# Optimization experiments

Measured on AMD Instinct MI355X. Metric: run time of the kernel, lower is better.

The kernel has to match this reference:

```python
import math
import jax, jax.numpy as jnp
import numpy as np

N_HEAD = 4
D_MODEL = 96
BS, N_TOK = 32, 512
A2LEN = 150          # a2len % 16 != 0 so padn > 0 (asserted in torch code)
DST_MXLEN = 32


def setup_inputs() -> dict:
    key = jax.random.key(0)
    k1, k2, k3, k4, k5, k6 = jax.random.split(key, 6)
    x = jax.random.normal(k1, (BS, N_TOK, D_MODEL), dtype=jnp.float32)
    # LinearM: w is [outdim, indim+1], last column is the bias, zeroed at init
    wqv_w = 0.02 * jax.random.normal(k2, (3 * D_MODEL, D_MODEL + 1), dtype=jnp.float32)
    wqv_w = wqv_w.at[:, -1].set(0.0)
    fanout_w = 0.02 * jax.random.normal(k3, (D_MODEL, D_MODEL + 1), dtype=jnp.float32)
    fanout_w = fanout_w.at[:, -1].set(0.0)

    def make_coo(k):
        # COO triples [dst, src, dst_cnt]; every dst has DST_MXLEN sources
        dst = jnp.repeat(jnp.arange(N_TOK), DST_MXLEN)
        src = jax.random.randint(k, (N_TOK * DST_MXLEN,), 0, N_TOK)
        cnt = jnp.tile(jnp.arange(DST_MXLEN), N_TOK)
        return jnp.stack([dst, src, cnt], axis=1).astype(jnp.int32)

    coo0 = make_coo(k4)
    coo1 = make_coo(k5)
    a2a = jnp.sort(jax.random.permutation(k6, N_TOK)[:A2LEN]).astype(jnp.int32)
    return {"x": x, "wqv_w": wqv_w, "fanout_w": fanout_w,
            "coo0": coo0, "coo1": coo1, "a2a": a2a, "dst_mxlen": DST_MXLEN}


def _linm(w, x):
    # LinearM: einsum('oi,bhi->bho') + bias column
    return jnp.einsum('oi,bti->bto', w[:, :-1], x) + w[:, -1]


def _l1attn_sparse(v, q, k, coo, dst_mxlen):
    # l1attn_sparse_cuda.L1AttnSparse: per-(dst,src) L1 scores scattered into a
    # [n_tok, dst_mxlen] ragged table (pad = -1e12), softmax over the fan-in slot.
    bs, n_tok, h, w = q.shape
    dst, src, cnt = coo[:, 0], coo[:, 1], coo[:, 2]
    scale = 1.0 / math.sqrt(w)
    ww = -jnp.sum(jnp.abs(q[:, dst] - k[:, src]), axis=-1) * scale    # [bs, cl, h]
    attn = jnp.full((bs, n_tok, dst_mxlen, h), -1e12, dtype=q.dtype)
    attn = attn.at[:, dst, cnt, :].set(ww)
    attn_sm = jax.nn.softmax(attn, axis=2)
    vw = jnp.zeros((bs, n_tok, dst_mxlen, h, w), dtype=q.dtype)
    vw = vw.at[:, dst, cnt, :, :].set(v[:, src])                      # gather by src
    return jnp.einsum('bdrh,bdrhw->bdhw', attn_sm, vw)


def _forward(x, wqv_w, fanout_w, coo0, coo1, a2a, dst_mxlen):
    bs, n_tok, width = x.shape
    h = N_HEAD
    y = _linm(wqv_w, x)
    q, k, v = jnp.split(y, 3, axis=-1)

    # --- dense all-to-all L1 attention on tokens a2a, channels 72:96 (h*6) ---
    a2len = a2a.shape[0]
    q1 = q[:, a2a, 72:].reshape(bs, a2len, h, 6)
    k1 = k[:, a2a, 72:].reshape(bs, a2len, h, 6)
    v1 = v[:, a2a, 72:].reshape(bs, a2len, h, 6)
    padl = (a2len + 15) // 16 * 16
    q2 = jnp.pad(q1, ((0, 0), (0, padl - a2len), (0, 0), (0, 0)))
    k2 = jnp.pad(k1, ((0, 0), (0, padl - a2len), (0, 0), (0, 0)))
    scale = 1.0 / math.sqrt(6)
    # l1attn_cuda.L1Attn: a[b, s, d, h] = -scale * sum_w |q[b,d,h,w] - k[b,s,h,w]|
    a = -jnp.sum(jnp.abs(q2[:, None, :, :, :] - k2[:, :, None, :, :]), axis=-1) * scale
    a = a[:, :a2len + 1, :a2len + 1, :]   # keep one zero-score pad row (attention sink)
    a = jax.nn.softmax(a, axis=1)         # softmax over src dim
    a = a[:, :a2len, :a2len, :]
    b1 = jnp.einsum('bsdh,bshw->bdhw', a, v1)
    b2 = jnp.zeros((bs, n_tok, h, 6), dtype=x.dtype).at[:, a2a].set(b1)
    dense = b2.reshape(bs, n_tok, h * 6)

    # --- two sparse COO L1-attention groups: channels 32:52 and 52:72 (h*5) ---
    sparse_out = []
    for i, coo in enumerate((coo0, coo1)):
        sta = 32 + 20 * i
        q1 = q[:, :, sta:sta + 20].reshape(bs, n_tok, h, 5)
        k1 = k[:, :, sta:sta + 20].reshape(bs, n_tok, h, 5)
        v1 = v[:, :, sta:sta + 20].reshape(bs, n_tok, h, 5)
        sparse_out.append(_l1attn_sparse(v1, q1, k1, coo, dst_mxlen).reshape(bs, n_tok, h * 5))

    # channels 0:32 are never written -> zeros
    b = jnp.concatenate([jnp.zeros((bs, n_tok, 32), dtype=x.dtype),
                         sparse_out[0], sparse_out[1], dense], axis=-1)
    yb = b * jax.nn.sigmoid(1.702 * b)    # QuickGELU
    return x + _linm(fanout_w, yb)


def reference(x, wqv_w, fanout_w, coo0, coo1, a2a, dst_mxlen):
    return _forward(x, wqv_w, fanout_w, coo0, coo1, a2a, dst_mxlen)
```

## Files before the change

### kernel.cpp

```cpp
#include <hip/hip_runtime.h>
#include <hip/hip_bf16.h>
#include <math.h>

#define BS    32
#define T     512
#define BT    (BS * T)
#define D     96
#define H     4
#define MX    32
#define A2MAX 160

#define QKV_TOK  16
#define FUSE_TOK 16

__device__ __forceinline__ int a2a_pos(const int* __restrict__ a2a, int n, int t) {
    int lo = 0, hi = n;
    while (lo < hi) { const int mid = (lo + hi) >> 1; if (a2a[mid] < t) lo = mid + 1; else hi = mid; }
    return (lo < n && a2a[lo] == t) ? lo : -1;
}

__global__ void prep_kernel(const float* __restrict__ wqv, const float* __restrict__ fw,
                            const int* __restrict__ coo0, const int* __restrict__ coo1,
                            int nedges,
                            float* __restrict__ WT, float* __restrict__ FWT,
                            int* __restrict__ srcs) {
    int idx = blockIdx.x * blockDim.x + threadIdx.x;
    if (idx < 97 * 192) {
        const int i = idx / 192, oc = idx - 192 * i;
        const int p = oc >> 6, c = oc & 63;
        WT[idx] = wqv[(p * 96 + 32 + c) * 97 + i];
        return;
    }
    idx -= 97 * 192;
    if (idx < 65 * 96) {
        const int i = idx / 96, o = idx - 96 * i;
        FWT[idx] = fw[o * 97 + 32 + i];
        return;
    }
    idx -= 65 * 96;
    if (idx < 2 * nedges) {
        const int ci = idx / nedges;
        const int e  = idx - ci * nedges;
        const int* row = (ci == 0 ? coo0 : coo1) + e * 3;
        const int dst = row[0], src = row[1], cnt = row[2];
        if (dst >= 0 && dst < T && cnt >= 0 && cnt < MX)
            srcs[(ci * T + dst) * MX + cnt] = src;
    }
}

__global__ void qkv_kernel(const float* __restrict__ x, const float* __restrict__ WT,
                           const int* __restrict__ a2a, int a2len,
                           float* __restrict__ QS, float* __restrict__ KS,
                           float* __restrict__ VS,
                           float* __restrict__ Qg, float* __restrict__ Kg,
                           float* __restrict__ Vg) {
    const int tid  = threadIdx.x;
    const int base = blockIdx.x * QKV_TOK;
    const int tloc = base & (T - 1);
    __shared__ float xs[QKV_TOK * D];
    __shared__ int   posA[QKV_TOK];
    float4* xs4 = (float4*)xs;
    const float4* xg = (const float4*)(x + base * D);
    xs4[tid]       = xg[tid];
    xs4[tid + 192] = xg[tid + 192];
    if (tid < QKV_TOK) posA[tid] = a2a_pos(a2a, a2len, tloc + tid);
    __syncthreads();
    float acc[QKV_TOK];
    const float bias = WT[96 * 192 + tid];
    #pragma unroll
    for (int j = 0; j < QKV_TOK; ++j) acc[j] = bias;
    #pragma unroll 3
    for (int i4 = 0; i4 < 24; ++i4) {
        const float w0 = WT[(4 * i4 + 0) * 192 + tid];
        const float w1 = WT[(4 * i4 + 1) * 192 + tid];
        const float w2 = WT[(4 * i4 + 2) * 192 + tid];
        const float w3 = WT[(4 * i4 + 3) * 192 + tid];
        #pragma unroll
        for (int j = 0; j < QKV_TOK; ++j) {
            const float4 xv = xs4[j * 24 + i4];
            acc[j] += w0 * xv.x + w1 * xv.y + w2 * xv.z + w3 * xv.w;
        }
    }
    const int part = tid >> 6, c = tid & 63;
    const int b    = base >> 9;
    if (c < 40) {
        float* XS = (part == 0) ? QS : (part == 1 ? KS : VS);
        float4* dp = (float4*)(XS + ((size_t)c * BS + b) * T + tloc);
        #pragma unroll
        for (int m = 0; m < 4; ++m)
            dp[m] = make_float4(acc[4 * m], acc[4 * m + 1],
                                acc[4 * m + 2], acc[4 * m + 3]);
    } else {
        float* g = (part == 0) ? Qg : (part == 1 ? Kg : Vg);
        #pragma unroll
        for (int j = 0; j < QKV_TOK; ++j) {
            const int ps = posA[j];
            if (ps >= 0) g[((size_t)b * A2MAX + ps) * 24 + (c - 40)] = acc[j];
        }
    }
}

__global__ void attn_kernel(const float* __restrict__ QS, const float* __restrict__ KS,
                            const float* __restrict__ VS, const int* __restrict__ srcs,
                            const float* __restrict__ Qg, const float* __restrict__ Kg,
                            const float* __restrict__ Vg, const int* __restrict__ a2a,
                            int a2len, int extra, float* __restrict__ B) {
    __shared__ float sm[A2MAX * 32 * 2];
    __shared__ int   rows[A2MAX];
    const int b   = blockIdx.y;
    const int tid = threadIdx.x;

    if (blockIdx.x < 8) {
        const int ci = blockIdx.x >> 2, h = blockIdx.x & 3;
        const int cb = 20 * ci + 5 * h;
        float* ks = sm;
        float* vs = sm + 5 * T;
        const size_t rowbase = ((size_t)cb * BS + b) * T;
        #pragma unroll
        for (int i = tid; i < 5 * T; i += 512) {
            const int w = i >> 9, s = i & (T - 1);
            ks[i] = KS[rowbase + (size_t)w * BS * T + s];
            vs[i] = VS[rowbase + (size_t)w * BS * T + s];
        }
        __syncthreads();
        const float iscale = 0.4472135954999579f;
        const int t = tid;
        const float q0 = QS[rowbase + 0 * BS * T + t];
        const float q1 = QS[rowbase + 1 * BS * T + t];
        const float q2 = QS[rowbase + 2 * BS * T + t];
        const float q3 = QS[rowbase + 3 * BS * T + t];
        const float q4 = QS[rowbase + 4 * BS * T + t];
        const int4* sp4 = (const int4*)(srcs + (ci * T + t) * MX);
        float l = 0.f, o0 = 0.f, o1 = 0.f, o2 = 0.f, o3 = 0.f, o4 = 0.f;
        #pragma unroll 2
        for (int c4 = 0; c4 < MX / 4; ++c4) {
            const int4 s4 = sp4[c4];
            const int sv[4] = {s4.x, s4.y, s4.z, s4.w};
            #pragma unroll
            for (int m = 0; m < 4; ++m) {
                const int s = sv[m];
                if (s < 0) continue;
                const float sum = fabsf(q0 - ks[s]) + fabsf(q1 - ks[T + s]) +
                                  fabsf(q2 - ks[2 * T + s]) + fabsf(q3 - ks[3 * T + s]) +
                                  fabsf(q4 - ks[4 * T + s]);
                const float e = __expf(-sum * iscale);
                l  += e;
                o0 += e * vs[s];         o1 += e * vs[T + s];
                o2 += e * vs[2 * T + s]; o3 += e * vs[3 * T + s];
                o4 += e * vs[4 * T + s];
            }
        }
        const float inv = (l > 0.f) ? 1.f / l : 0.f;
        float* bp = B + ((size_t)b * T + t) * 96 + 32 + cb;
        bp[0] = o0 * inv; bp[1] = o1 * inv; bp[2] = o2 * inv;
        bp[3] = o3 * inv; bp[4] = o4 * inv;
    } else {
        const int tile = blockIdx.x - 8;
        float* ks = sm;
        float* vs = sm + A2MAX * 32;
        for (int i = tid; i < a2len; i += 512) rows[i] = a2a[i];
        const int nq = (a2len * 24) / 4;
        const float4* kg4 = (const float4*)(Kg + (size_t)b * A2MAX * 24);
        const float4* vg4 = (const float4*)(Vg + (size_t)b * A2MAX * 24);
        for (int idx = tid; idx < nq; idx += 512) {
            const int s = idx / 6, r = idx - 6 * s;
            const float4 kk = kg4[idx];
            const float4 vv = vg4[idx];
            const float kv[4]  = {kk.x, kk.y, kk.z, kk.w};
            const float vv4[4] = {vv.x, vv.y, vv.z, vv.w};
            #pragma unroll
            for (int m = 0; m < 4; ++m) {
                const int w = r * 4 + m, hh = w / 6, ww = w - 6 * hh;
                ks[s * 32 + hh * 8 + ww] = kv[m];
                vs[s * 32 + hh * 8 + ww] = vv4[m];
            }
        }
        __syncthreads();
        const int h = tid & 3, dl = tid >> 2;
        const int d = tile * 128 + dl;
        if (d >= a2len) return;
        const float scale = 0.4082482904638631f;
        const float* qp = Qg + ((size_t)b * A2MAX + d) * 24 + h * 6;
        const float q0 = qp[0], q1 = qp[1], q2 = qp[2],
                    q3 = qp[3], q4 = qp[4], q5 = qp[5];
        float l = 0.f, o0 = 0.f, o1 = 0.f, o2 = 0.f, o3 = 0.f, o4 = 0.f, o5 = 0.f;
        for (int s = 0; s < a2len; ++s) {
            const float4 k4 = *(const float4*)&ks[s * 32 + h * 8];
            const float2 k2 = *(const float2*)&ks[s * 32 + h * 8 + 4];
            const float sum = fabsf(q0 - k4.x) + fabsf(q1 - k4.y) + fabsf(q2 - k4.z) +
                              fabsf(q3 - k4.w) + fabsf(q4 - k2.x) + fabsf(q5 - k2.y);
            const float e = __expf(-sum * scale);
            const float4 v4 = *(const float4*)&vs[s * 32 + h * 8];
            const float2 v2 = *(const float2*)&vs[s * 32 + h * 8 + 4];
            l  += e;
            o0 += e * v4.x; o1 += e * v4.y; o2 += e * v4.z;
            o3 += e * v4.w; o4 += e * v2.x; o5 += e * v2.y;
        }
        if (extra) {
            const float sum = fabsf(q0) + fabsf(q1) + fabsf(q2) +
                              fabsf(q3) + fabsf(q4) + fabsf(q5);
            l += __expf(-sum * scale);
        }
        const float inv = 1.f / l;
        float* bp = B + ((size_t)b * T + rows[d]) * 96 + 72 + h * 6;
        bp[0] = o0 * inv; bp[1] = o1 * inv; bp[2] = o2 * inv;
        bp[3] = o3 * inv; bp[4] = o4 * inv; bp[5] = o5 * inv;
    }
}

__global__ void fuse_kernel(const float* __restrict__ x, const float* __restrict__ FWT,
                            const float* __restrict__ B, const int* __restrict__ a2a,
                            int a2len, float* __restrict__ out) {
    const int tid  = threadIdx.x;
    const int half = tid / 96;
    const int o    = tid - 96 * half;
    const int base = blockIdx.x * FUSE_TOK;
    const int tloc = base & (T - 1);
    __shared__ float yb[FUSE_TOK * 64];
    __shared__ int   maskA[FUSE_TOK];
    float4* yb4 = (float4*)yb;
    if (tid < FUSE_TOK) maskA[tid] = a2a_pos(a2a, a2len, tloc + tid);
    __syncthreads();
    for (int idx = tid; idx < FUSE_TOK * 64; idx += 192) {
        const int j = idx >> 6, k = idx & 63;
        float v = B[(base + j) * 96 + 32 + k];
        if (k >= 40 && maskA[j] < 0) v = 0.f;
        yb[idx] = v / (1.f + __expf(-1.702f * v));
    }
    __syncthreads();
    float acc[FUSE_TOK / 2];
    const float bias = FWT[64 * 96 + o];
    #pragma unroll
    for (int j = 0; j < FUSE_TOK / 2; ++j) acc[j] = bias;
    #pragma unroll 2
    for (int i4 = 0; i4 < 16; ++i4) {
        const float w0 = FWT[(4 * i4 + 0) * 96 + o];
        const float w1 = FWT[(4 * i4 + 1) * 96 + o];
        const float w2 = FWT[(4 * i4 + 2) * 96 + o];
        const float w3 = FWT[(4 * i4 + 3) * 96 + o];
        #pragma unroll
        for (int j = 0; j < FUSE_TOK / 2; ++j) {
            const float4 yv = yb4[(2 * j + half) * 16 + i4];
            acc[j] += w0 * yv.x + w1 * yv.y + w2 * yv.z + w3 * yv.w;
        }
    }
    #pragma unroll
    for (int j = 0; j < FUSE_TOK / 2; ++j) {
        const int token = base + 2 * j + half;
        out[token * D + o] = x[token * D + o] + acc[j];
    }
}

extern "C" void kernel_launch(void* const* d_in, const int* in_sizes, int n_in,
                              void* d_out, int out_size, void* d_ws, size_t ws_size,
                              hipStream_t stream) {
    const float* x   = (const float*)d_in[0];
    const float* wqv = (const float*)d_in[1];
    const float* fw  = (const float*)d_in[2];
    const int*  coo0 = (const int*)d_in[3];
    const int*  coo1 = (const int*)d_in[4];
    const int*  a2a  = (const int*)d_in[5];
    int a2len        = in_sizes[5];
    if (a2len > A2MAX) a2len = A2MAX;
    const int nedges = in_sizes[3] / 3;

    float* QS  = (float*)d_ws;
    float* KS  = QS + (size_t)40 * BS * T;
    float* VS  = KS + (size_t)40 * BS * T;
    float* Bb  = VS + (size_t)40 * BS * T;
    float* Qg  = Bb + (size_t)BT * 96;
    float* Kg  = Qg + (size_t)BS * A2MAX * 24;
    float* Vg  = Kg + (size_t)BS * A2MAX * 24;
    int*  srcs = (int*)(Vg + (size_t)BS * A2MAX * 24);
    float* WT  = (float*)(srcs + 2 * T * MX);
    float* FWT = WT + 97 * 192;

    const int prep_n = 97 * 192 + 65 * 96 + 2 * nedges;
    prep_kernel<<<(prep_n + 255) / 256, 256, 0, stream>>>(
        wqv, fw, coo0, coo1, nedges, WT, FWT, srcs);
    qkv_kernel<<<BT / QKV_TOK, 192, 0, stream>>>(x, WT, a2a, a2len,
                                                 QS, KS, VS, Qg, Kg, Vg);
    const int padl  = (a2len + 15) / 16 * 16;
    const int extra = (padl > a2len) ? 1 : 0;
    attn_kernel<<<dim3(8 + (a2len + 127) / 128, BS), 512, 0, stream>>>(
        QS, KS, VS, srcs, Qg, Kg, Vg, a2a, a2len, extra, Bb);
    fuse_kernel<<<BT / FUSE_TOK, 192, 0, stream>>>(x, FWT, Bb, a2a, a2len, (float*)d_out);
}
```

Measured before the change: 134.8 us.

## Split fused attention kernel into separate sparse and dense kernels

```diff
diff --git a/kernel.cpp b/kernel.cpp
--- a/kernel.cpp
+++ b/kernel.cpp
@@ -12,6 +12,7 @@
 
 #define QKV_TOK  16
 #define FUSE_TOK 16
+#define DT       32
 
 __device__ __forceinline__ int a2a_pos(const int* __restrict__ a2a, int n, int t) {
     int lo = 0, hi = n;
@@ -100,112 +101,113 @@
     }
 }
 
-__global__ void attn_kernel(const float* __restrict__ QS, const float* __restrict__ KS,
-                            const float* __restrict__ VS, const int* __restrict__ srcs,
-                            const float* __restrict__ Qg, const float* __restrict__ Kg,
-                            const float* __restrict__ Vg, const int* __restrict__ a2a,
-                            int a2len, int extra, float* __restrict__ B) {
-    __shared__ float sm[A2MAX * 32 * 2];
+__global__ void sparse_kernel(const float* __restrict__ QS, const float* __restrict__ KS,
+                              const float* __restrict__ VS, const int* __restrict__ srcs,
+                              float* __restrict__ B) {
+    const int b   = blockIdx.y;
+    const int ci  = blockIdx.x >> 2, h = blockIdx.x & 3;
+    const int cb  = 20 * ci + 5 * h;
+    const int tid = threadIdx.x;
+    __shared__ float ks[5 * T];
+    __shared__ float vs[5 * T];
+    const size_t rowbase = ((size_t)cb * BS + b) * T;
+    #pragma unroll
+    for (int i = tid; i < 5 * T; i += 512) {
+        const int w = i >> 9, s = i & (T - 1);
+        ks[i] = KS[rowbase + (size_t)w * BS * T + s];
+        vs[i] = VS[rowbase + (size_t)w * BS * T + s];
+    }
+    __syncthreads();
+    const float iscale = 0.4472135954999579f;
+    const int t = tid;
+    const float q0 = QS[rowbase + 0 * BS * T + t];
+    const float q1 = QS[rowbase + 1 * BS * T + t];
+    const float q2 = QS[rowbase + 2 * BS * T + t];
+    const float q3 = QS[rowbase + 3 * BS * T + t];
+    const float q4 = QS[rowbase + 4 * BS * T + t];
+    const int4* sp4 = (const int4*)(srcs + (ci * T + t) * MX);
+    float l = 0.f, o0 = 0.f, o1 = 0.f, o2 = 0.f, o3 = 0.f, o4 = 0.f;
+    #pragma unroll 2
+    for (int c4 = 0; c4 < MX / 4; ++c4) {
+        const int4 s4 = sp4[c4];
+        const int sv[4] = {s4.x, s4.y, s4.z, s4.w};
+        #pragma unroll
+        for (int m = 0; m < 4; ++m) {
+            const int s = sv[m];
+            if (s < 0) continue;
+            const float sum = fabsf(q0 - ks[s]) + fabsf(q1 - ks[T + s]) +
+                              fabsf(q2 - ks[2 * T + s]) + fabsf(q3 - ks[3 * T + s]) +
+                              fabsf(q4 - ks[4 * T + s]);
+            const float e = __expf(-sum * iscale);
+            l  += e;
+            o0 += e * vs[s];         o1 += e * vs[T + s];
+            o2 += e * vs[2 * T + s]; o3 += e * vs[3 * T + s];
+            o4 += e * vs[4 * T + s];
+        }
+    }
+    const float inv = (l > 0.f) ? 1.f / l : 0.f;
+    float* bp = B + ((size_t)b * T + t) * 96 + 32 + cb;
+    bp[0] = o0 * inv; bp[1] = o1 * inv; bp[2] = o2 * inv;
+    bp[3] = o3 * inv; bp[4] = o4 * inv;
+}
+
+__global__ void dense_kernel(const float* __restrict__ Qg,
+                             const float* __restrict__ Kg, const float* __restrict__ Vg,
+                             const int* __restrict__ a2a,
+                             int a2len, int extra, float* __restrict__ B) {
+    const int b   = blockIdx.y;
+    const int d0  = blockIdx.x * DT;
+    const int tid = threadIdx.x;
     __shared__ int   rows[A2MAX];
-    const int b   = blockIdx.y;
-    const int tid = threadIdx.x;
-
-    if (blockIdx.x < 8) {
-        const int ci = blockIdx.x >> 2, h = blockIdx.x & 3;
-        const int cb = 20 * ci + 5 * h;
-        float* ks = sm;
-        float* vs = sm + 5 * T;
-        const size_t rowbase = ((size_t)cb * BS + b) * T;
-        #pragma unroll
-        for (int i = tid; i < 5 * T; i += 512) {
-            const int w = i >> 9, s = i & (T - 1);
-            ks[i] = KS[rowbase + (size_t)w * BS * T + s];
-            vs[i] = VS[rowbase + (size_t)w * BS * T + s];
-        }
-        __syncthreads();
-        const float iscale = 0.4472135954999579f;
-        const int t = tid;
-        const float q0 = QS[rowbase + 0 * BS * T + t];
-        const float q1 = QS[rowbase + 1 * BS * T + t];
-        const float q2 = QS[rowbase + 2 * BS * T + t];
-        const float q3 = QS[rowbase + 3 * BS * T + t];
-        const float q4 = QS[rowbase + 4 * BS * T + t];
-        const int4* sp4 = (const int4*)(srcs + (ci * T + t) * MX);
-        float l = 0.f, o0 = 0.f, o1 = 0.f, o2 = 0.f, o3 = 0.f, o4 = 0.f;
-        #pragma unroll 2
-        for (int c4 = 0; c4 < MX / 4; ++c4) {
-            const int4 s4 = sp4[c4];
-            const int sv[4] = {s4.x, s4.y, s4.z, s4.w};
-            #pragma unroll
-            for (int m = 0; m < 4; ++m) {
-                const int s = sv[m];
-                if (s < 0) continue;
-                const float sum = fabsf(q0 - ks[s]) + fabsf(q1 - ks[T + s]) +
-                                  fabsf(q2 - ks[2 * T + s]) + fabsf(q3 - ks[3 * T + s]) +
-                                  fabsf(q4 - ks[4 * T + s]);
-                const float e = __expf(-sum * iscale);
-                l  += e;
-                o0 += e * vs[s];         o1 += e * vs[T + s];
-                o2 += e * vs[2 * T + s]; o3 += e * vs[3 * T + s];
-                o4 += e * vs[4 * T + s];
-            }
-        }
-        const float inv = (l > 0.f) ? 1.f / l : 0.f;
-        float* bp = B + ((size_t)b * T + t) * 96 + 32 + cb;
-        bp[0] = o0 * inv; bp[1] = o1 * inv; bp[2] = o2 * inv;
-        bp[3] = o3 * inv; bp[4] = o4 * inv;
-    } else {
-        const int tile = blockIdx.x - 8;
-        float* ks = sm;
-        float* vs = sm + A2MAX * 32;
-        for (int i = tid; i < a2len; i += 512) rows[i] = a2a[i];
-        const int nq = (a2len * 24) / 4;
-        const float4* kg4 = (const float4*)(Kg + (size_t)b * A2MAX * 24);
-        const float4* vg4 = (const float4*)(Vg + (size_t)b * A2MAX * 24);
-        for (int idx = tid; idx < nq; idx += 512) {
-            const int s = idx / 6, r = idx - 6 * s;
-            const float4 kk = kg4[idx];
-            const float4 vv = vg4[idx];
-            const float kv[4]  = {kk.x, kk.y, kk.z, kk.w};
-            const float vv4[4] = {vv.x, vv.y, vv.z, vv.w};
-            #pragma unroll
-            for (int m = 0; m < 4; ++m) {
-                const int w = r * 4 + m, hh = w / 6, ww = w - 6 * hh;
-                ks[s * 32 + hh * 8 + ww] = kv[m];
-                vs[s * 32 + hh * 8 + ww] = vv4[m];
-            }
-        }
-        __syncthreads();
-        const int h = tid & 3, dl = tid >> 2;
-        const int d = tile * 128 + dl;
-        if (d >= a2len) return;
-        const float scale = 0.4082482904638631f;
-        const float* qp = Qg + ((size_t)b * A2MAX + d) * 24 + h * 6;
-        const float q0 = qp[0], q1 = qp[1], q2 = qp[2],
-                    q3 = qp[3], q4 = qp[4], q5 = qp[5];
-        float l = 0.f, o0 = 0.f, o1 = 0.f, o2 = 0.f, o3 = 0.f, o4 = 0.f, o5 = 0.f;
-        for (int s = 0; s < a2len; ++s) {
-            const float4 k4 = *(const float4*)&ks[s * 32 + h * 8];
-            const float2 k2 = *(const float2*)&ks[s * 32 + h * 8 + 4];
-            const float sum = fabsf(q0 - k4.x) + fabsf(q1 - k4.y) + fabsf(q2 - k4.z) +
-                              fabsf(q3 - k4.w) + fabsf(q4 - k2.x) + fabsf(q5 - k2.y);
-            const float e = __expf(-sum * scale);
-            const float4 v4 = *(const float4*)&vs[s * 32 + h * 8];
-            const float2 v2 = *(const float2*)&vs[s * 32 + h * 8 + 4];
-            l  += e;
-            o0 += e * v4.x; o1 += e * v4.y; o2 += e * v4.z;
-            o3 += e * v4.w; o4 += e * v2.x; o5 += e * v2.y;
-        }
-        if (extra) {
-            const float sum = fabsf(q0) + fabsf(q1) + fabsf(q2) +
-                              fabsf(q3) + fabsf(q4) + fabsf(q5);
-            l += __expf(-sum * scale);
-        }
-        const float inv = 1.f / l;
-        float* bp = B + ((size_t)b * T + rows[d]) * 96 + 72 + h * 6;
-        bp[0] = o0 * inv; bp[1] = o1 * inv; bp[2] = o2 * inv;
-        bp[3] = o3 * inv; bp[4] = o4 * inv; bp[5] = o5 * inv;
-    }
+    __shared__ float ks[A2MAX * 32];
+    __shared__ float vs[A2MAX * 32];
+    for (int i = tid; i < a2len; i += 128) rows[i] = a2a[i];
+    const int nq = (a2len * 24) / 4;
+    const float4* kg4 = (const float4*)(Kg + (size_t)b * A2MAX * 24);
+    const float4* vg4 = (const float4*)(Vg + (size_t)b * A2MAX * 24);
+    for (int idx = tid; idx < nq; idx += 128) {
+        const int s = idx / 6, r = idx - 6 * s;
+        const float4 kk = kg4[idx];
+        const float4 vv = vg4[idx];
+        const float kv[4]  = {kk.x, kk.y, kk.z, kk.w};
+        const float vv4[4] = {vv.x, vv.y, vv.z, vv.w};
+        #pragma unroll
+        for (int m = 0; m < 4; ++m) {
+            const int w = r * 4 + m, hh = w / 6, ww = w - 6 * hh;
+            ks[s * 32 + hh * 8 + ww] = kv[m];
+            vs[s * 32 + hh * 8 + ww] = vv4[m];
+        }
+    }
+    __syncthreads();
+    const int h = tid & 3, dl = tid >> 2;
+    const int d = d0 + dl;
+    if (d >= a2len) return;
+    const float scale = 0.4082482904638631f;
+    const float* qp = Qg + ((size_t)b * A2MAX + d) * 24 + h * 6;
+    const float q0 = qp[0], q1 = qp[1], q2 = qp[2],
+                q3 = qp[3], q4 = qp[4], q5 = qp[5];
+    float l = 0.f, o0 = 0.f, o1 = 0.f, o2 = 0.f, o3 = 0.f, o4 = 0.f, o5 = 0.f;
+    for (int s = 0; s < a2len; ++s) {
+        const float4 k4 = *(const float4*)&ks[s * 32 + h * 8];
+        const float2 k2 = *(const float2*)&ks[s * 32 + h * 8 + 4];
+        const float sum = fabsf(q0 - k4.x) + fabsf(q1 - k4.y) + fabsf(q2 - k4.z) +
+                          fabsf(q3 - k4.w) + fabsf(q4 - k2.x) + fabsf(q5 - k2.y);
+        const float e = __expf(-sum * scale);
+        const float4 v4 = *(const float4*)&vs[s * 32 + h * 8];
+        const float2 v2 = *(const float2*)&vs[s * 32 + h * 8 + 4];
+        l  += e;
+        o0 += e * v4.x; o1 += e * v4.y; o2 += e * v4.z;
+        o3 += e * v4.w; o4 += e * v2.x; o5 += e * v2.y;
+    }
+    if (extra) {
+        const float sum = fabsf(q0) + fabsf(q1) + fabsf(q2) +
+                          fabsf(q3) + fabsf(q4) + fabsf(q5);
+        l += __expf(-sum * scale);
+    }
+    const float inv = 1.f / l;
+    float* bp = B + ((size_t)b * T + rows[d]) * 96 + 72 + h * 6;
+    bp[0] = o0 * inv; bp[1] = o1 * inv; bp[2] = o2 * inv;
+    bp[3] = o3 * inv; bp[4] = o4 * inv; bp[5] = o5 * inv;
 }
 
 __global__ void fuse_kernel(const float* __restrict__ x, const float* __restrict__ FWT,
@@ -280,9 +282,10 @@
         wqv, fw, coo0, coo1, nedges, WT, FWT, srcs);
     qkv_kernel<<<BT / QKV_TOK, 192, 0, stream>>>(x, WT, a2a, a2len,
                                                  QS, KS, VS, Qg, Kg, Vg);
+    sparse_kernel<<<dim3(8, BS), 512, 0, stream>>>(QS, KS, VS, srcs, Bb);
     const int padl  = (a2len + 15) / 16 * 16;
     const int extra = (padl > a2len) ? 1 : 0;
-    attn_kernel<<<dim3(8 + (a2len + 127) / 128, BS), 512, 0, stream>>>(
-        QS, KS, VS, srcs, Qg, Kg, Vg, a2a, a2len, extra, Bb);
+    dense_kernel<<<dim3((a2len + DT - 1) / DT, BS), 128, 0, stream>>>(
+        Qg, Kg, Vg, a2a, a2len, extra, Bb);
     fuse_kernel<<<BT / FUSE_TOK, 192, 0, stream>>>(x, FWT, Bb, a2a, a2len, (float*)d_out);
 }
```

After: 134.2 us. No clear change (-0.5%).
